# Performance work log

Hardware: AMD Instinct MI355X
Metric: run time of the kernel (lower is better)

## Reference

```python
import jax, jax.numpy as jnp
import numpy as np

TEMPERATURE = 0.07
NEG_INF = -9e15
EPS = 1e-12

def setup_inputs() -> dict:
    key = jax.random.key(0)
    k1, k2 = jax.random.split(key)
    N, D = 8192, 128
    features = jax.random.normal(k1, (N, D), dtype=jnp.float32)
    labels = jax.random.randint(k2, (N,), 0, 16, dtype=jnp.int64)
    return {"features": features, "labels": labels}

def reference(features, labels):
    N = features.shape[0]
    # L2 normalize rows (torch F.normalize: x / max(||x||, eps))
    norm = jnp.linalg.norm(features, axis=1, keepdims=True)
    f = features / jnp.maximum(norm, EPS)
    # [N, N] similarity
    sim = jnp.matmul(f, f.T) / TEMPERATURE
    eye = jnp.eye(N, dtype=bool)
    sim = jnp.where(eye, NEG_INF, sim)
    # positive-pair mask: same label, excluding self
    pos_mask = ((labels[:, None] == labels[None, :]) & ~eye).astype(sim.dtype)
    denom = jnp.exp(sim).sum(axis=1, keepdims=True)  # [N, 1]
    log_prob = sim - jnp.log(denom + EPS)
    loss = -(pos_mask * log_prob).sum(axis=1) / (pos_mask.sum(axis=1) + EPS)
    return loss.mean()
```

## Files before the change

kernel.cpp:

```cpp
#include <hip/hip_runtime.h>
#include <hip/hip_bf16.h>

#define EPS 1e-12f
#define SQRT_C_EXP 4.53981597f
#define M_LN2F 0.69314718056f

#define BM 256
#define BN 128
#define KD 128
#define NCHUNK 8
#define NPART 16
#define PSTRIDE 48

typedef __attribute__((ext_vector_type(4))) float f32x4;
typedef __attribute__((ext_vector_type(8))) short bf16x8;

__device__ __forceinline__ float bf2f(ushort u) {
    unsigned int x = ((unsigned int)u) << 16;
    return __uint_as_float(x);
}

__device__ __forceinline__ void gload16(const void* g, void* l) {
    __builtin_amdgcn_global_load_lds(
        (const __attribute__((address_space(1))) void*)g,
        (__attribute__((address_space(3))) void*)l, 16, 0, 0);
}

__device__ __forceinline__ const bf16x8* lds_frag(const ushort* base, int r, int slot) {
    int sw = slot ^ (r & 7);
    return reinterpret_cast<const bf16x8*>(
        reinterpret_cast<const char*>(base) + r * 256 + sw * 16);
}

__global__ void normalize_kernel(const float* __restrict__ feat,
                                 ushort* __restrict__ fb,
                                 float* __restrict__ sq,
                                 int N) {
    int r    = (blockIdx.x * blockDim.x + threadIdx.x) >> 6;
    int lane = threadIdx.x & 63;
    if (r >= N) return;
    const float2 v = *reinterpret_cast<const float2*>(feat + (size_t)r * KD + lane * 2);
    float s = v.x * v.x + v.y * v.y;
    #pragma unroll
    for (int off = 1; off < 64; off <<= 1) s += __shfl_xor(s, off);
    const float scale = SQRT_C_EXP / fmaxf(sqrtf(s), EPS);

    __hip_bfloat16 h0 = __float2bfloat16(v.x * scale);
    __hip_bfloat16 h1 = __float2bfloat16(v.y * scale);
    ushort u0 = *reinterpret_cast<ushort*>(&h0);
    ushort u1 = *reinterpret_cast<ushort*>(&h1);
    unsigned int pack = (unsigned int)u0 | ((unsigned int)u1 << 16);
    *reinterpret_cast<unsigned int*>(fb + (size_t)r * KD + lane * 2) = pack;

    float q0 = bf2f(u0), q1 = bf2f(u1);
    float q = q0 * q0 + q1 * q1;
    #pragma unroll
    for (int off = 1; off < 64; off <<= 1) q += __shfl_xor(q, off);
    if (lane == 0) sq[r] = q;
}

__global__ __launch_bounds__(512, 2) void supcon_denom(
    const ushort* __restrict__ fb,
    const int* __restrict__ labels,
    float* __restrict__ part,
    int N) {

    __shared__ __align__(16) ushort As[BM * KD];
    __shared__ __align__(16) ushort Bs[2][BN * KD];

    const int tid  = threadIdx.x;
    const int lane = tid & 63;
    const int w    = tid >> 6;
    const int wr   = w >> 1;
    const int wc   = w & 1;
    const int r16  = lane & 15;
    const int g4   = lane >> 4;

    const int rowbase = blockIdx.y * BM;
    const int col0    = blockIdx.x * (BN * NCHUNK);

    {
        const ushort* gA = fb + (size_t)rowbase * KD;
        #pragma unroll
        for (int i = 0; i < 8; i++) {
            int d = i * 512 + tid;
            int s = d ^ ((d >> 4) & 7);
            gload16(gA + (size_t)s * 8, &As[d * 8]);
        }
        const ushort* gB = fb + (size_t)col0 * KD;
        #pragma unroll
        for (int i = 0; i < 4; i++) {
            int d = i * 512 + tid;
            int s = d ^ ((d >> 4) & 7);
            gload16(gB + (size_t)s * 8, &Bs[0][d * 8]);
        }
    }

    int rlab[4][4];
    #pragma unroll
    for (int m = 0; m < 4; m++)
        #pragma unroll
        for (int i = 0; i < 4; i++)
            rlab[m][i] = labels[rowbase + wr * 64 + m * 16 + g4 * 4 + i];

    __syncthreads();

    bf16x8 a[4][4];
    #pragma unroll
    for (int ks = 0; ks < 4; ks++) {
        const int slot = ks * 4 + g4;
        #pragma unroll
        for (int m = 0; m < 4; m++)
            a[ks][m] = *lds_frag(As, wr * 64 + m * 16 + r16, slot);
    }

    float pd[4][4], pp[4][4], pc[4][4];
    #pragma unroll
    for (int m = 0; m < 4; m++)
        #pragma unroll
        for (int i = 0; i < 4; i++) { pd[m][i] = 0.f; pp[m][i] = 0.f; pc[m][i] = 0.f; }

    int cur = 0;
    for (int c = 0; c < NCHUNK; c++) {
        if (c + 1 < NCHUNK) {
            const ushort* gB = fb + (size_t)(col0 + (c + 1) * BN) * KD;
            ushort* dstb = Bs[cur ^ 1];
            #pragma unroll
            for (int i = 0; i < 4; i++) {
                int d = i * 512 + tid;
                int s = d ^ ((d >> 4) & 7);
                gload16(gB + (size_t)s * 8, &dstb[d * 8]);
            }
        }

        const ushort* bbase = Bs[cur];
        const int colbase = col0 + c * BN + wc * 64;

        #pragma unroll 1
        for (int n = 0; n < 4; n++) {
            const int clab = labels[colbase + n * 16 + r16];

            f32x4 acc[4];
            #pragma unroll
            for (int m = 0; m < 4; m++) acc[m] = f32x4{0.f, 0.f, 0.f, 0.f};

            #pragma unroll
            for (int ks = 0; ks < 4; ks++) {
                const int slot = ks * 4 + g4;
                bf16x8 bv = *lds_frag(bbase, wc * 64 + n * 16 + r16, slot);
                #pragma unroll
                for (int m = 0; m < 4; m++)
                    acc[m] = __builtin_amdgcn_mfma_f32_16x16x32_bf16(a[ks][m], bv, acc[m], 0, 0, 0);
            }

            #pragma unroll
            for (int m = 0; m < 4; m++)
                #pragma unroll
                for (int i = 0; i < 4; i++) {
                    const float sim = acc[m][i];
                    pd[m][i] += __builtin_amdgcn_exp2f(sim);
                    const bool mt = (rlab[m][i] == clab);
                    pp[m][i] += mt ? sim : 0.f;
                    pc[m][i] += mt ? 1.f : 0.f;
                }
        }

        __syncthreads();
        cur ^= 1;
    }

    #pragma unroll
    for (int off = 1; off < 16; off <<= 1)
        #pragma unroll
        for (int m = 0; m < 4; m++)
            #pragma unroll
            for (int i = 0; i < 4; i++) {
                pd[m][i] += __shfl_xor(pd[m][i], off);
                pp[m][i] += __shfl_xor(pp[m][i], off);
                pc[m][i] += __shfl_xor(pc[m][i], off);
            }

    if (r16 == 0) {
        const int slot = blockIdx.x * 2 + wc;
        #pragma unroll
        for (int m = 0; m < 4; m++)
            #pragma unroll
            for (int i = 0; i < 4; i++) {
                int r = rowbase + wr * 64 + m * 16 + g4 * 4 + i;
                float* p = part + (size_t)r * PSTRIDE + slot;
                p[0]  = pd[m][i];
                p[16] = pp[m][i];
                p[32] = pc[m][i];
            }
    }
}

__global__ void rowloss_kernel(const float* __restrict__ part,
                               const float* __restrict__ sq,
                               float* __restrict__ rowloss,
                               int N) {
    int r    = (blockIdx.x * blockDim.x + threadIdx.x) >> 6;
    int lane = threadIdx.x & 63;
    if (r >= N) return;

    float v = (lane < PSTRIDE) ? part[(size_t)r * PSTRIDE + lane] : 0.f;
    #pragma unroll
    for (int off = 1; off < 16; off <<= 1) v += __shfl_xor(v, off);
    float dsum = __shfl(v, 0);
    float psum = __shfl(v, 16);
    float csum = __shfl(v, 32);

    if (lane == 0) {
        float sqr    = sq[r];
        float possum = (psum - sqr) * M_LN2F;
        float cnt    = csum - 1.0f;
        float dn     = dsum - __builtin_amdgcn_exp2f(sqr);
        rowloss[r]   = -(possum - cnt * logf(dn + EPS)) / (cnt + EPS);
    }
}

__global__ void reduce_kernel(const float* __restrict__ rowloss,
                              float* __restrict__ out, int N) {
    __shared__ float sdata[16];
    float s = 0.f;
    for (int r = threadIdx.x; r < N; r += blockDim.x) s += rowloss[r];
    #pragma unroll
    for (int off = 1; off < 64; off <<= 1) s += __shfl_xor(s, off);
    int wv = threadIdx.x >> 6;
    if ((threadIdx.x & 63) == 0) sdata[wv] = s;
    __syncthreads();
    if (threadIdx.x == 0) {
        float t = 0.f;
        int nw = (int)(blockDim.x >> 6);
        for (int i = 0; i < nw; i++) t += sdata[i];
        out[0] = t / (float)N;
    }
}

extern "C" void kernel_launch(void* const* d_in, const int* in_sizes, int n_in,
                              void* d_out, int out_size, void* d_ws, size_t ws_size,
                              hipStream_t stream) {
    const float* feat = (const float*)d_in[0];
    const int* labels = (const int*)d_in[1];
    const int N = in_sizes[1];

    char* ws = (char*)d_ws;
    size_t off = 0;
    ushort* fb     = (ushort*)(ws + off);  off += (size_t)N * KD * sizeof(ushort);
    float* sq      = (float*)(ws + off);   off += (size_t)N * sizeof(float);
    float* part    = (float*)(ws + off);   off += (size_t)N * PSTRIDE * sizeof(float);
    float* rowloss = (float*)(ws + off);

    normalize_kernel<<<(N + 3) / 4, 256, 0, stream>>>(feat, fb, sq, N);

    dim3 grid(N / (BN * NCHUNK), N / BM);
    supcon_denom<<<grid, 512, 0, stream>>>(fb, labels, part, N);

    rowloss_kernel<<<(N + 3) / 4, 256, 0, stream>>>(part, sq, rowloss, N);
    reduce_kernel<<<1, 1024, 0, stream>>>(rowloss, (float*)d_out, N);
}
```

Before: 48.63 us.

## Drop LDS staging in favor of per-wave direct global loads; hoist class counts

The similarity kernel stops staging A and B tiles in shared memory. Each wave now loads its own 64-row A fragments and streams 16-column B fragments straight from global memory into registers, prefetching one step ahead, and the grid is split into 32 column groups. Per-row positive counts are no longer accumulated in the inner loop. A 16-class label histogram is computed once in the normalize kernel and looked up in the row-loss kernel. This removes LDS traffic, barriers and a compare/add per element, but relies on L2 and cache hits for B reuse, since each wave re-reads columns with no sharing inside the block, and it hardcodes 16 classes.

```diff
diff --git a/kernel.cpp b/kernel.cpp
--- a/kernel.cpp
+++ b/kernel.cpp
@@ -4,13 +4,11 @@
 #define EPS 1e-12f
 #define SQRT_C_EXP 4.53981597f
 #define M_LN2F 0.69314718056f
-
-#define BM 256
-#define BN 128
+#define NUM_CLASSES 16
+
 #define KD 128
-#define NCHUNK 8
-#define NPART 16
-#define PSTRIDE 48
+#define NCOLG 32
+#define PSTRIDE 64
 
 typedef __attribute__((ext_vector_type(4))) float f32x4;
 typedef __attribute__((ext_vector_type(8))) short bf16x8;
@@ -20,153 +18,149 @@
     return __uint_as_float(x);
 }
 
-__device__ __forceinline__ void gload16(const void* g, void* l) {
-    __builtin_amdgcn_global_load_lds(
-        (const __attribute__((address_space(1))) void*)g,
-        (__attribute__((address_space(3))) void*)l, 16, 0, 0);
-}
-
-__device__ __forceinline__ const bf16x8* lds_frag(const ushort* base, int r, int slot) {
-    int sw = slot ^ (r & 7);
-    return reinterpret_cast<const bf16x8*>(
-        reinterpret_cast<const char*>(base) + r * 256 + sw * 16);
-}
-
 __global__ void normalize_kernel(const float* __restrict__ feat,
+                                 const int* __restrict__ labels,
                                  ushort* __restrict__ fb,
                                  float* __restrict__ sq,
+                                 float* __restrict__ cnt16,
                                  int N) {
-    int r    = (blockIdx.x * blockDim.x + threadIdx.x) >> 6;
-    int lane = threadIdx.x & 63;
-    if (r >= N) return;
-    const float2 v = *reinterpret_cast<const float2*>(feat + (size_t)r * KD + lane * 2);
-    float s = v.x * v.x + v.y * v.y;
-    #pragma unroll
-    for (int off = 1; off < 64; off <<= 1) s += __shfl_xor(s, off);
-    const float scale = SQRT_C_EXP / fmaxf(sqrtf(s), EPS);
-
-    __hip_bfloat16 h0 = __float2bfloat16(v.x * scale);
-    __hip_bfloat16 h1 = __float2bfloat16(v.y * scale);
-    ushort u0 = *reinterpret_cast<ushort*>(&h0);
-    ushort u1 = *reinterpret_cast<ushort*>(&h1);
-    unsigned int pack = (unsigned int)u0 | ((unsigned int)u1 << 16);
-    *reinterpret_cast<unsigned int*>(fb + (size_t)r * KD + lane * 2) = pack;
-
-    float q0 = bf2f(u0), q1 = bf2f(u1);
-    float q = q0 * q0 + q1 * q1;
-    #pragma unroll
-    for (int off = 1; off < 64; off <<= 1) q += __shfl_xor(q, off);
-    if (lane == 0) sq[r] = q;
-}
-
-__global__ __launch_bounds__(512, 2) void supcon_denom(
+    const int tid  = threadIdx.x;
+    const int lane = tid & 63;
+    const int w    = tid >> 6;
+    int r = (blockIdx.x * blockDim.x + tid) >> 6;
+    if (r < N) {
+        const float2 v = *reinterpret_cast<const float2*>(feat + (size_t)r * KD + lane * 2);
+        float s = v.x * v.x + v.y * v.y;
+        #pragma unroll
+        for (int off = 1; off < 64; off <<= 1) s += __shfl_xor(s, off);
+        const float scale = SQRT_C_EXP / fmaxf(sqrtf(s), EPS);
+
+        __hip_bfloat16 h0 = __float2bfloat16(v.x * scale);
+        __hip_bfloat16 h1 = __float2bfloat16(v.y * scale);
+        ushort u0 = *reinterpret_cast<ushort*>(&h0);
+        ushort u1 = *reinterpret_cast<ushort*>(&h1);
+        unsigned int pack = (unsigned int)u0 | ((unsigned int)u1 << 16);
+        *reinterpret_cast<unsigned int*>(fb + (size_t)r * KD + lane * 2) = pack;
+
+        float q0 = bf2f(u0), q1 = bf2f(u1);
+        float q = q0 * q0 + q1 * q1;
+        #pragma unroll
+        for (int off = 1; off < 64; off <<= 1) q += __shfl_xor(q, off);
+        if (lane == 0) sq[r] = q;
+    }
+
+    if (blockIdx.x == 0) {
+        int cl[NUM_CLASSES];
+        #pragma unroll
+        for (int c = 0; c < NUM_CLASSES; c++) cl[c] = 0;
+        for (int i = tid; i < N; i += 256) {
+            int lb = labels[i];
+            #pragma unroll
+            for (int c = 0; c < NUM_CLASSES; c++) cl[c] += (lb == c) ? 1 : 0;
+        }
+        #pragma unroll
+        for (int c = 0; c < NUM_CLASSES; c++) {
+            int v = cl[c];
+            #pragma unroll
+            for (int off = 1; off < 64; off <<= 1) v += __shfl_xor(v, off);
+            cl[c] = v;
+        }
+        __shared__ int hw[4][NUM_CLASSES];
+        if (lane == 0) {
+            #pragma unroll
+            for (int c = 0; c < NUM_CLASSES; c++) hw[w][c] = cl[c];
+        }
+        __syncthreads();
+        if (tid < NUM_CLASSES)
+            cnt16[tid] = (float)(hw[0][tid] + hw[1][tid] + hw[2][tid] + hw[3][tid]);
+    }
+}
+
+__global__ __launch_bounds__(256, 2) void supcon_denom(
     const ushort* __restrict__ fb,
     const int* __restrict__ labels,
     float* __restrict__ part,
     int N) {
 
-    __shared__ __align__(16) ushort As[BM * KD];
-    __shared__ __align__(16) ushort Bs[2][BN * KD];
-
     const int tid  = threadIdx.x;
     const int lane = tid & 63;
     const int w    = tid >> 6;
-    const int wr   = w >> 1;
-    const int wc   = w & 1;
     const int r16  = lane & 15;
     const int g4   = lane >> 4;
-
-    const int rowbase = blockIdx.y * BM;
-    const int col0    = blockIdx.x * (BN * NCHUNK);
-
-    {
-        const ushort* gA = fb + (size_t)rowbase * KD;
-        #pragma unroll
-        for (int i = 0; i < 8; i++) {
-            int d = i * 512 + tid;
-            int s = d ^ ((d >> 4) & 7);
-            gload16(gA + (size_t)s * 8, &As[d * 8]);
-        }
-        const ushort* gB = fb + (size_t)col0 * KD;
-        #pragma unroll
-        for (int i = 0; i < 4; i++) {
-            int d = i * 512 + tid;
-            int s = d ^ ((d >> 4) & 7);
-            gload16(gB + (size_t)s * 8, &Bs[0][d * 8]);
-        }
-    }
-
+    const int kg8  = g4 << 3;
+
+    const int wid      = blockIdx.x * 4 + w;
+    const int rowgroup = wid >> 5;
+    const int colgroup = wid & (NCOLG - 1);
+    const int rowbase  = rowgroup * 64;
+    const int colsper  = N / NCOLG;
+    const int col0     = colgroup * colsper;
+    const int nstep    = colsper >> 4;
+
+    bf16x8 a[4][4];
+    #pragma unroll
+    for (int ks = 0; ks < 4; ks++) {
+        const int kk = ks * 32 + kg8;
+        #pragma unroll
+        for (int m = 0; m < 4; m++)
+            a[ks][m] = *reinterpret_cast<const bf16x8*>(
+                fb + (size_t)(rowbase + m * 16 + r16) * KD + kk);
+    }
     int rlab[4][4];
     #pragma unroll
     for (int m = 0; m < 4; m++)
         #pragma unroll
         for (int i = 0; i < 4; i++)
-            rlab[m][i] = labels[rowbase + wr * 64 + m * 16 + g4 * 4 + i];
-
-    __syncthreads();
-
-    bf16x8 a[4][4];
-    #pragma unroll
-    for (int ks = 0; ks < 4; ks++) {
-        const int slot = ks * 4 + g4;
-        #pragma unroll
-        for (int m = 0; m < 4; m++)
-            a[ks][m] = *lds_frag(As, wr * 64 + m * 16 + r16, slot);
-    }
-
-    float pd[4][4], pp[4][4], pc[4][4];
+            rlab[m][i] = labels[rowbase + m * 16 + g4 * 4 + i];
+
+    float pd[4][4], pp[4][4];
     #pragma unroll
     for (int m = 0; m < 4; m++)
         #pragma unroll
-        for (int i = 0; i < 4; i++) { pd[m][i] = 0.f; pp[m][i] = 0.f; pc[m][i] = 0.f; }
-
-    int cur = 0;
-    for (int c = 0; c < NCHUNK; c++) {
-        if (c + 1 < NCHUNK) {
-            const ushort* gB = fb + (size_t)(col0 + (c + 1) * BN) * KD;
-            ushort* dstb = Bs[cur ^ 1];
+        for (int i = 0; i < 4; i++) { pd[m][i] = 0.f; pp[m][i] = 0.f; }
+
+    bf16x8 bvc[4];
+    #pragma unroll
+    for (int ks = 0; ks < 4; ks++)
+        bvc[ks] = *reinterpret_cast<const bf16x8*>(
+            fb + (size_t)(col0 + r16) * KD + ks * 32 + kg8);
+    int clab_c = labels[col0 + r16];
+
+    #pragma unroll 1
+    for (int s = 0; s < nstep; s++) {
+        bf16x8 bvn[4];
+        int clab_n = 0;
+        if (s + 1 < nstep) {
+            const int cb = col0 + (s + 1) * 16 + r16;
+            #pragma unroll
+            for (int ks = 0; ks < 4; ks++)
+                bvn[ks] = *reinterpret_cast<const bf16x8*>(
+                    fb + (size_t)cb * KD + ks * 32 + kg8);
+            clab_n = labels[cb];
+        }
+
+        f32x4 acc[4];
+        #pragma unroll
+        for (int m = 0; m < 4; m++) acc[m] = f32x4{0.f, 0.f, 0.f, 0.f};
+
+        #pragma unroll
+        for (int ks = 0; ks < 4; ks++)
+            #pragma unroll
+            for (int m = 0; m < 4; m++)
+                acc[m] = __builtin_amdgcn_mfma_f32_16x16x32_bf16(a[ks][m], bvc[ks], acc[m], 0, 0, 0);
+
+        #pragma unroll
+        for (int m = 0; m < 4; m++)
             #pragma unroll
             for (int i = 0; i < 4; i++) {
-                int d = i * 512 + tid;
-                int s = d ^ ((d >> 4) & 7);
-                gload16(gB + (size_t)s * 8, &dstb[d * 8]);
+                const float sim = acc[m][i];
+                pd[m][i] += __builtin_amdgcn_exp2f(sim);
+                pp[m][i] += (rlab[m][i] == clab_c) ? sim : 0.f;
             }
-        }
-
-        const ushort* bbase = Bs[cur];
-        const int colbase = col0 + c * BN + wc * 64;
-
-        #pragma unroll 1
-        for (int n = 0; n < 4; n++) {
-            const int clab = labels[colbase + n * 16 + r16];
-
-            f32x4 acc[4];
-            #pragma unroll
-            for (int m = 0; m < 4; m++) acc[m] = f32x4{0.f, 0.f, 0.f, 0.f};
-
-            #pragma unroll
-            for (int ks = 0; ks < 4; ks++) {
-                const int slot = ks * 4 + g4;
-                bf16x8 bv = *lds_frag(bbase, wc * 64 + n * 16 + r16, slot);
-                #pragma unroll
-                for (int m = 0; m < 4; m++)
-                    acc[m] = __builtin_amdgcn_mfma_f32_16x16x32_bf16(a[ks][m], bv, acc[m], 0, 0, 0);
-            }
-
-            #pragma unroll
-            for (int m = 0; m < 4; m++)
-                #pragma unroll
-                for (int i = 0; i < 4; i++) {
-                    const float sim = acc[m][i];
-                    pd[m][i] += __builtin_amdgcn_exp2f(sim);
-                    const bool mt = (rlab[m][i] == clab);
-                    pp[m][i] += mt ? sim : 0.f;
-                    pc[m][i] += mt ? 1.f : 0.f;
-                }
-        }
-
-        __syncthreads();
-        cur ^= 1;
+
+        #pragma unroll
+        for (int ks = 0; ks < 4; ks++) bvc[ks] = bvn[ks];
+        clab_c = clab_n;
     }
 
     #pragma unroll
@@ -177,43 +171,41 @@
             for (int i = 0; i < 4; i++) {
                 pd[m][i] += __shfl_xor(pd[m][i], off);
                 pp[m][i] += __shfl_xor(pp[m][i], off);
-                pc[m][i] += __shfl_xor(pc[m][i], off);
             }
 
     if (r16 == 0) {
-        const int slot = blockIdx.x * 2 + wc;
         #pragma unroll
         for (int m = 0; m < 4; m++)
             #pragma unroll
             for (int i = 0; i < 4; i++) {
-                int r = rowbase + wr * 64 + m * 16 + g4 * 4 + i;
-                float* p = part + (size_t)r * PSTRIDE + slot;
+                int r = rowbase + m * 16 + g4 * 4 + i;
+                float* p = part + (size_t)r * PSTRIDE + colgroup;
                 p[0]  = pd[m][i];
-                p[16] = pp[m][i];
-                p[32] = pc[m][i];
+                p[32] = pp[m][i];
             }
     }
 }
 
 __global__ void rowloss_kernel(const float* __restrict__ part,
                                const float* __restrict__ sq,
+                               const int* __restrict__ labels,
+                               const float* __restrict__ cnt16,
                                float* __restrict__ rowloss,
                                int N) {
     int r    = (blockIdx.x * blockDim.x + threadIdx.x) >> 6;
     int lane = threadIdx.x & 63;
     if (r >= N) return;
 
-    float v = (lane < PSTRIDE) ? part[(size_t)r * PSTRIDE + lane] : 0.f;
-    #pragma unroll
-    for (int off = 1; off < 16; off <<= 1) v += __shfl_xor(v, off);
+    float v = part[(size_t)r * PSTRIDE + lane];
+    #pragma unroll
+    for (int off = 1; off < 32; off <<= 1) v += __shfl_xor(v, off);
     float dsum = __shfl(v, 0);
-    float psum = __shfl(v, 16);
-    float csum = __shfl(v, 32);
+    float psum = __shfl(v, 32);
 
     if (lane == 0) {
         float sqr    = sq[r];
         float possum = (psum - sqr) * M_LN2F;
-        float cnt    = csum - 1.0f;
+        float cnt    = cnt16[labels[r]] - 1.0f;
         float dn     = dsum - __builtin_amdgcn_exp2f(sqr);
         rowloss[r]   = -(possum - cnt * logf(dn + EPS)) / (cnt + EPS);
     }
@@ -248,14 +240,14 @@
     size_t off = 0;
     ushort* fb     = (ushort*)(ws + off);  off += (size_t)N * KD * sizeof(ushort);
     float* sq      = (float*)(ws + off);   off += (size_t)N * sizeof(float);
+    float* cnt16   = (float*)(ws + off);   off += (size_t)NUM_CLASSES * sizeof(float);
     float* part    = (float*)(ws + off);   off += (size_t)N * PSTRIDE * sizeof(float);
     float* rowloss = (float*)(ws + off);
 
-    normalize_kernel<<<(N + 3) / 4, 256, 0, stream>>>(feat, fb, sq, N);
-
-    dim3 grid(N / (BN * NCHUNK), N / BM);
-    supcon_denom<<<grid, 512, 0, stream>>>(fb, labels, part, N);
-
-    rowloss_kernel<<<(N + 3) / 4, 256, 0, stream>>>(part, sq, rowloss, N);
+    normalize_kernel<<<(N + 3) / 4, 256, 0, stream>>>(feat, labels, fb, sq, cnt16, N);
+
+    supcon_denom<<<(N / 64) * NCOLG / 4, 256, 0, stream>>>(fb, labels, part, N);
+
+    rowloss_kernel<<<(N + 3) / 4, 256, 0, stream>>>(part, sq, labels, cnt16, rowloss, N);
     reduce_kernel<<<1, 1024, 0, stream>>>(rowloss, (float*)d_out, N);
 }
```

Result: slower. 65.74 us (+35.2%).
